# Performance work log

Measured on AMD Instinct MI355X. Metric: run time of the kernel, lower is better.

Reference implementation:

```python
import jax, jax.numpy as jnp
import numpy as np

E, H, I, T = 8, 1024, 4096, 8192  # experts, hidden, intermediate, total tokens


def setup_inputs() -> dict:
    key = jax.random.key(0)
    k1, k2, k3 = jax.random.split(key, 3)
    hiddens = jax.random.normal(k1, (T, H), dtype=jnp.float32)
    # expert weights, scaled like standard init
    w1_weight = jax.random.normal(k2, (E, H, I), dtype=jnp.float32) * (1.0 / np.sqrt(H).astype(np.float32))
    w2_weight = jax.random.normal(k3, (E, I, H), dtype=jnp.float32) * (1.0 / np.sqrt(I).astype(np.float32))
    # tokens are pre-grouped by expert; equal load of T//E tokens per expert
    batch_sizes = jnp.full((E,), T // E, dtype=jnp.int32)
    return {"hiddens": hiddens, "batch_sizes": batch_sizes,
            "w1_weight": w1_weight, "w2_weight": w2_weight}


def _gmm(x, w, batch_sizes):
    """Grouped matmul: rows of x are grouped contiguously by expert.
    x: [T, K], w: [E, K, N], batch_sizes: [E] (sums to T). Returns [T, N].
    Loop is over the small fixed expert count; each iteration is a dense
    GEMM with rows outside the expert's segment masked to zero.
    """
    n_experts = w.shape[0]
    ends = jnp.cumsum(batch_sizes)
    starts = ends - batch_sizes
    tok = jnp.arange(x.shape[0])[:, None]  # [T, 1]
    out = jnp.zeros((x.shape[0], w.shape[2]), dtype=x.dtype)
    for e in range(n_experts):
        mask = (tok >= starts[e]) & (tok < ends[e])  # [T, 1]
        out = out + jnp.where(mask, x, jnp.zeros((), x.dtype)) @ w[e]
    return out


def reference(hiddens, batch_sizes, w1_weight, w2_weight):
    up = _gmm(hiddens, w1_weight, batch_sizes)    # [T, I]
    down = _gmm(up, w2_weight, batch_sizes)       # [T, H]
    return down
```

## Files before the change

### kernel.cpp

```cpp
#include <hip/hip_runtime.h>
#include <hip/hip_bf16.h>


typedef unsigned short u16;
typedef unsigned int u32;
typedef __attribute__((ext_vector_type(8))) short bf16x8;
typedef __attribute__((ext_vector_type(4))) float f32x4;
typedef __attribute__((ext_vector_type(4))) u32 u32x4;

#define E_N 8
#define H_N 1024
#define I_N 4096
#define T_N 8192

#define GLD2LDS16(g, l)                                                        \
  __builtin_amdgcn_global_load_lds(                                            \
      (const __attribute__((address_space(1))) void*)(g),                      \
      (__attribute__((address_space(3))) void*)(l), 16, 0, 0)

__device__ __forceinline__ u16 f2bf(float f) {
  __hip_bfloat16 h = __float2bfloat16(f);
  return *(reinterpret_cast<u16*>(&h));
}

__device__ __forceinline__ u32 pkbf(float lo, float hi) {
  u32 a = __float_as_uint(lo) + 0x8000u;
  u32 b = __float_as_uint(hi) + 0x8000u;
  return __builtin_amdgcn_perm(b, a, 0x07060302u);
}

__global__ __launch_bounds__(256) void wgemm_kernel(const float* __restrict__ w1,
                                                    const float* __restrict__ w2,
                                                    u16* __restrict__ mt) {
  __shared__ u16 ldsA[4096];
  __shared__ u16 ldsB[4096];

  const int tid = threadIdx.x;
  const int lane = tid & 63;
  const int wv = tid >> 6;
  const int wm = wv >> 1, wn = wv & 1;
  const int lm = lane & 15, quad = lane >> 4;

  const int e = blockIdx.y;
  const int bm = blockIdx.x >> 3, bn = blockIdx.x & 7;
  const int row0 = bm * 128;
  const int col0 = bn * 128;

  const float* w1e = w1 + (size_t)e * H_N * I_N;
  const float* w2e = w2 + (size_t)e * I_N * H_N;
  u16* mte = mt + (size_t)e * H_N * H_N;

  const int a_mp = lane * 2;
  const float* gA0 = w2e + (size_t)(8 * wv) * H_N + row0 + a_mp;

  const int b_r = tid >> 2;
  const int b_k = (tid & 3) * 8;
  const float* gB0 = w1e + (size_t)(col0 + b_r) * I_N + b_k;
  const float* gB1 = gB0 + (size_t)64 * I_N;
  u16* ldsB_w = ldsB + b_r * 32 + b_k;

  f32x4 acc[4][4];
#pragma unroll
  for (int i = 0; i < 4; i++)
#pragma unroll
    for (int j = 0; j < 4; j++) acc[i][j] = (f32x4){0.f, 0.f, 0.f, 0.f};

  for (int k0 = 0; k0 < I_N; k0 += 32) {
    float2 va[8];
    const float* gA = gA0 + (size_t)k0 * H_N;
#pragma unroll
    for (int kk = 0; kk < 8; kk++)
      va[kk] = *(const float2*)(gA + (size_t)kk * H_N);

    float4 f0 = *(const float4*)(gB0 + k0);
    float4 f1 = *(const float4*)(gB0 + k0 + 4);
    float4 f2 = *(const float4*)(gB1 + k0);
    float4 f3 = *(const float4*)(gB1 + k0 + 4);

    u32 evn[4], odd[4];
#pragma unroll
    for (int j = 0; j < 4; j++) {
      evn[j] = pkbf(va[2 * j].x, va[2 * j + 1].x);
      odd[j] = pkbf(va[2 * j].y, va[2 * j + 1].y);
    }
    *(u32x4*)(ldsA + wv * 1024 + a_mp * 8) =
        (u32x4){evn[0], evn[1], evn[2], evn[3]};
    *(u32x4*)(ldsA + wv * 1024 + (a_mp + 1) * 8) =
        (u32x4){odd[0], odd[1], odd[2], odd[3]};

    *(u32x4*)ldsB_w = (u32x4){pkbf(f0.x, f0.y), pkbf(f0.z, f0.w),
                              pkbf(f1.x, f1.y), pkbf(f1.z, f1.w)};
    *(u32x4*)(ldsB_w + 64 * 32) = (u32x4){pkbf(f2.x, f2.y), pkbf(f2.z, f2.w),
                                          pkbf(f3.x, f3.y), pkbf(f3.z, f3.w)};

    __syncthreads();

    bf16x8 af[4], bfr[4];
#pragma unroll
    for (int mi = 0; mi < 4; mi++)
      af[mi] = *(const bf16x8*)(ldsA + quad * 1024 + (wm * 64 + mi * 16 + lm) * 8);
#pragma unroll
    for (int ni = 0; ni < 4; ni++)
      bfr[ni] = *(const bf16x8*)(ldsB + (wn * 64 + ni * 16 + lm) * 32 + quad * 8);
#pragma unroll
    for (int mi = 0; mi < 4; mi++)
#pragma unroll
      for (int ni = 0; ni < 4; ni++)
        acc[mi][ni] = __builtin_amdgcn_mfma_f32_16x16x32_bf16(
            af[mi], bfr[ni], acc[mi][ni], 0, 0, 0);

    __syncthreads();
  }

  const int orow = row0 + wm * 64 + quad * 4;
  const int ocol = col0 + wn * 64 + lm;
#pragma unroll
  for (int mi = 0; mi < 4; mi++)
#pragma unroll
    for (int ni = 0; ni < 4; ni++)
#pragma unroll
      for (int r = 0; r < 4; r++)
        mte[(size_t)(orow + mi * 16 + r) * H_N + ocol + ni * 16] =
            f2bf(acc[mi][ni][r]);
}

__global__ __launch_bounds__(256) void tgemm_kernel(const float* __restrict__ x,
                                                    const int* __restrict__ bsz,
                                                    const u16* __restrict__ mt,
                                                    float* __restrict__ out) {
  __shared__ u16 ldsA[4096];
  __shared__ u16 ldsB[4096];

  const int tid = threadIdx.x;
  const int lane = tid & 63;
  const int wv = tid >> 6;
  const int wm = wv >> 1, wn = wv & 1;
  const int lm = lane & 15, quad = lane >> 4;

  const int bm = blockIdx.x >> 3, bn = blockIdx.x & 7;
  const int row0 = bm * 128;
  const int col0 = bn * 128;

  int e = 0, start = 0;
#pragma unroll
  for (int i = 0; i < E_N; i++) {
    int b = bsz[i];
    if (row0 >= start + b) { start += b; e = i + 1; }
  }
  const u16* mte = mt + (size_t)e * H_N * H_N;

  const int s_r = tid >> 2;
  const int s_k = (tid & 3) * 8;
  const float* gA0 = x + (size_t)(row0 + s_r) * H_N + s_k;
  const float* gA1 = gA0 + (size_t)64 * H_N;
  const u16* gB0 = mte + (size_t)(col0 + s_r) * H_N + s_k;
  const u16* gB1 = gB0 + (size_t)64 * H_N;
  u16* ldsA_w = ldsA + s_r * 32 + s_k;
  u16* ldsB_dst = ldsB + wv * 512;

  f32x4 acc[4][4];
#pragma unroll
  for (int i = 0; i < 4; i++)
#pragma unroll
    for (int j = 0; j < 4; j++) acc[i][j] = (f32x4){0.f, 0.f, 0.f, 0.f};

  for (int k0 = 0; k0 < H_N; k0 += 32) {
    GLD2LDS16(gB0 + k0, ldsB_dst);
    GLD2LDS16(gB1 + k0, ldsB_dst + 2048);

    float4 f0 = *(const float4*)(gA0 + k0);
    float4 f1 = *(const float4*)(gA0 + k0 + 4);
    float4 f2 = *(const float4*)(gA1 + k0);
    float4 f3 = *(const float4*)(gA1 + k0 + 4);
    *(u32x4*)ldsA_w = (u32x4){pkbf(f0.x, f0.y), pkbf(f0.z, f0.w),
                              pkbf(f1.x, f1.y), pkbf(f1.z, f1.w)};
    *(u32x4*)(ldsA_w + 64 * 32) = (u32x4){pkbf(f2.x, f2.y), pkbf(f2.z, f2.w),
                                          pkbf(f3.x, f3.y), pkbf(f3.z, f3.w)};

    __syncthreads();

    bf16x8 af[4], bfr[4];
#pragma unroll
    for (int mi = 0; mi < 4; mi++)
      af[mi] = *(const bf16x8*)(ldsA + (wm * 64 + mi * 16 + lm) * 32 + quad * 8);
#pragma unroll
    for (int ni = 0; ni < 4; ni++)
      bfr[ni] = *(const bf16x8*)(ldsB + (wn * 64 + ni * 16 + lm) * 32 + quad * 8);
#pragma unroll
    for (int mi = 0; mi < 4; mi++)
#pragma unroll
      for (int ni = 0; ni < 4; ni++)
        acc[mi][ni] = __builtin_amdgcn_mfma_f32_16x16x32_bf16(
            af[mi], bfr[ni], acc[mi][ni], 0, 0, 0);

    __syncthreads();
  }

  const int orow = row0 + wm * 64 + quad * 4;
  const int ocol = col0 + wn * 64 + lm;
#pragma unroll
  for (int mi = 0; mi < 4; mi++)
#pragma unroll
    for (int ni = 0; ni < 4; ni++)
#pragma unroll
      for (int r = 0; r < 4; r++)
        out[(size_t)(orow + mi * 16 + r) * H_N + ocol + ni * 16] =
            acc[mi][ni][r];
}

extern "C" void kernel_launch(void* const* d_in, const int* in_sizes, int n_in,
                              void* d_out, int out_size, void* d_ws,
                              size_t ws_size, hipStream_t stream) {
  (void)in_sizes; (void)n_in; (void)out_size; (void)ws_size;
  const float* hiddens = (const float*)d_in[0];
  const int* bsz = (const int*)d_in[1];
  const float* w1 = (const float*)d_in[2];
  const float* w2 = (const float*)d_in[3];
  float* out = (float*)d_out;
  u16* mt = (u16*)d_ws;

  wgemm_kernel<<<dim3(64, E_N), 256, 0, stream>>>(w1, w2, mt);
  tgemm_kernel<<<dim3(512), 256, 0, stream>>>(hiddens, bsz, mt, out);
}
```

Before: 487.3 us.

## Pre-convert weights and activations to bf16 and use direct global-to-LDS loads

Adds separate conversion kernels that turn w1 and hiddens into bf16 and transpose-convert w2 into a K-contiguous bf16 layout in workspace. Both GEMM kernels can then load A and B tiles with global_load_lds instead of loading fp32 through registers and packing in the main loop. This removes repeated fp32 reads (each weight tile was re-read by 8 blocks) and in-loop conversion work. In exchange it adds three extra launches and a full fp32 read plus bf16 write of all weights per call, and it needs roughly 160 MB of workspace.

```diff
diff --git a/kernel.cpp b/kernel.cpp
--- a/kernel.cpp
+++ b/kernel.cpp
@@ -18,19 +18,68 @@
       (const __attribute__((address_space(1))) void*)(g),                      \
       (__attribute__((address_space(3))) void*)(l), 16, 0, 0)
 
-__device__ __forceinline__ u16 f2bf(float f) {
-  __hip_bfloat16 h = __float2bfloat16(f);
-  return *(reinterpret_cast<u16*>(&h));
-}
-
 __device__ __forceinline__ u32 pkbf(float lo, float hi) {
   u32 a = __float_as_uint(lo) + 0x8000u;
   u32 b = __float_as_uint(hi) + 0x8000u;
   return __builtin_amdgcn_perm(b, a, 0x07060302u);
 }
 
-__global__ __launch_bounds__(256) void wgemm_kernel(const float* __restrict__ w1,
-                                                    const float* __restrict__ w2,
+__device__ __forceinline__ u16 f2bf(float f) {
+  __hip_bfloat16 h = __float2bfloat16(f);
+  return *(reinterpret_cast<u16*>(&h));
+}
+
+__global__ __launch_bounds__(256) void cvt_kernel(const float* __restrict__ src,
+                                                  u16* __restrict__ dst) {
+  const size_t i = ((size_t)blockIdx.x * 256 + threadIdx.x) * 8;
+  float4 a = *(const float4*)(src + i);
+  float4 b = *(const float4*)(src + i + 4);
+  *(u32x4*)(dst + i) = (u32x4){pkbf(a.x, a.y), pkbf(a.z, a.w),
+                               pkbf(b.x, b.y), pkbf(b.z, b.w)};
+}
+
+__global__ __launch_bounds__(256) void transp_kernel(const float* __restrict__ w2,
+                                                     u16* __restrict__ w2t) {
+  __shared__ float tile[64 * 65];
+  const int tid = threadIdx.x;
+  const int h0 = blockIdx.x * 64;
+  const int i0 = blockIdx.y * 64;
+  const float* src = w2 + (size_t)blockIdx.z * I_N * H_N;
+  u16* dst = w2t + (size_t)blockIdx.z * H_N * I_N;
+
+  {
+    const int r = tid >> 4;
+    const int c4 = (tid & 15) * 4;
+#pragma unroll
+    for (int rr = 0; rr < 4; rr++) {
+      const int row = rr * 16 + r;
+      float4 v = *(const float4*)(src + (size_t)(i0 + row) * H_N + h0 + c4);
+      tile[row * 65 + c4 + 0] = v.x;
+      tile[row * 65 + c4 + 1] = v.y;
+      tile[row * 65 + c4 + 2] = v.z;
+      tile[row * 65 + c4 + 3] = v.w;
+    }
+  }
+  __syncthreads();
+
+  {
+    const int hr = tid >> 3;
+    const int ic = (tid & 7) * 8;
+#pragma unroll
+    for (int hh = 0; hh < 2; hh++) {
+      const int h = hh * 32 + hr;
+      u32 p[4];
+#pragma unroll
+      for (int j = 0; j < 4; j++)
+        p[j] = pkbf(tile[(ic + 2 * j) * 65 + h], tile[(ic + 2 * j + 1) * 65 + h]);
+      *(u32x4*)(dst + (size_t)(h0 + h) * I_N + i0 + ic) =
+          (u32x4){p[0], p[1], p[2], p[3]};
+    }
+  }
+}
+
+__global__ __launch_bounds__(256) void wgemm_kernel(const u16* __restrict__ w2t,
+                                                    const u16* __restrict__ w1b,
                                                     u16* __restrict__ mt) {
   __shared__ u16 ldsA[4096];
   __shared__ u16 ldsB[4096];
@@ -41,23 +90,23 @@
   const int wm = wv >> 1, wn = wv & 1;
   const int lm = lane & 15, quad = lane >> 4;
 
-  const int e = blockIdx.y;
-  const int bm = blockIdx.x >> 3, bn = blockIdx.x & 7;
-  const int row0 = bm * 128;
-  const int col0 = bn * 128;
-
-  const float* w1e = w1 + (size_t)e * H_N * I_N;
-  const float* w2e = w2 + (size_t)e * I_N * H_N;
+  const int e = blockIdx.x >> 6;
+  const int t = blockIdx.x & 63;
+  const int row0 = (t >> 3) * 128;
+  const int col0 = (t & 7) * 128;
+
+  const u16* Ae = w2t + (size_t)e * H_N * I_N;
+  const u16* Be = w1b + (size_t)e * H_N * I_N;
   u16* mte = mt + (size_t)e * H_N * H_N;
 
-  const int a_mp = lane * 2;
-  const float* gA0 = w2e + (size_t)(8 * wv) * H_N + row0 + a_mp;
-
-  const int b_r = tid >> 2;
-  const int b_k = (tid & 3) * 8;
-  const float* gB0 = w1e + (size_t)(col0 + b_r) * I_N + b_k;
-  const float* gB1 = gB0 + (size_t)64 * I_N;
-  u16* ldsB_w = ldsB + b_r * 32 + b_k;
+  const int s_r = tid >> 2;
+  const int s_k = (tid & 3) * 8;
+  const u16* gA0 = Ae + (size_t)(row0 + s_r) * I_N + s_k;
+  const u16* gA1 = gA0 + (size_t)64 * I_N;
+  const u16* gB0 = Be + (size_t)(col0 + s_r) * I_N + s_k;
+  const u16* gB1 = gB0 + (size_t)64 * I_N;
+  u16* ldsA_dst = ldsA + wv * 512;
+  u16* ldsB_dst = ldsB + wv * 512;
 
   f32x4 acc[4][4];
 #pragma unroll
@@ -66,39 +115,17 @@
     for (int j = 0; j < 4; j++) acc[i][j] = (f32x4){0.f, 0.f, 0.f, 0.f};
 
   for (int k0 = 0; k0 < I_N; k0 += 32) {
-    float2 va[8];
-    const float* gA = gA0 + (size_t)k0 * H_N;
-#pragma unroll
-    for (int kk = 0; kk < 8; kk++)
-      va[kk] = *(const float2*)(gA + (size_t)kk * H_N);
-
-    float4 f0 = *(const float4*)(gB0 + k0);
-    float4 f1 = *(const float4*)(gB0 + k0 + 4);
-    float4 f2 = *(const float4*)(gB1 + k0);
-    float4 f3 = *(const float4*)(gB1 + k0 + 4);
-
-    u32 evn[4], odd[4];
-#pragma unroll
-    for (int j = 0; j < 4; j++) {
-      evn[j] = pkbf(va[2 * j].x, va[2 * j + 1].x);
-      odd[j] = pkbf(va[2 * j].y, va[2 * j + 1].y);
-    }
-    *(u32x4*)(ldsA + wv * 1024 + a_mp * 8) =
-        (u32x4){evn[0], evn[1], evn[2], evn[3]};
-    *(u32x4*)(ldsA + wv * 1024 + (a_mp + 1) * 8) =
-        (u32x4){odd[0], odd[1], odd[2], odd[3]};
-
-    *(u32x4*)ldsB_w = (u32x4){pkbf(f0.x, f0.y), pkbf(f0.z, f0.w),
-                              pkbf(f1.x, f1.y), pkbf(f1.z, f1.w)};
-    *(u32x4*)(ldsB_w + 64 * 32) = (u32x4){pkbf(f2.x, f2.y), pkbf(f2.z, f2.w),
-                                          pkbf(f3.x, f3.y), pkbf(f3.z, f3.w)};
+    GLD2LDS16(gA0 + k0, ldsA_dst);
+    GLD2LDS16(gA1 + k0, ldsA_dst + 2048);
+    GLD2LDS16(gB0 + k0, ldsB_dst);
+    GLD2LDS16(gB1 + k0, ldsB_dst + 2048);
 
     __syncthreads();
 
     bf16x8 af[4], bfr[4];
 #pragma unroll
     for (int mi = 0; mi < 4; mi++)
-      af[mi] = *(const bf16x8*)(ldsA + quad * 1024 + (wm * 64 + mi * 16 + lm) * 8);
+      af[mi] = *(const bf16x8*)(ldsA + (wm * 64 + mi * 16 + lm) * 32 + quad * 8);
 #pragma unroll
     for (int ni = 0; ni < 4; ni++)
       bfr[ni] = *(const bf16x8*)(ldsB + (wn * 64 + ni * 16 + lm) * 32 + quad * 8);
@@ -124,7 +151,7 @@
             f2bf(acc[mi][ni][r]);
 }
 
-__global__ __launch_bounds__(256) void tgemm_kernel(const float* __restrict__ x,
+__global__ __launch_bounds__(256) void tgemm_kernel(const u16* __restrict__ xb,
                                                     const int* __restrict__ bsz,
                                                     const u16* __restrict__ mt,
                                                     float* __restrict__ out) {
@@ -151,11 +178,11 @@
 
   const int s_r = tid >> 2;
   const int s_k = (tid & 3) * 8;
-  const float* gA0 = x + (size_t)(row0 + s_r) * H_N + s_k;
-  const float* gA1 = gA0 + (size_t)64 * H_N;
+  const u16* gA0 = xb + (size_t)(row0 + s_r) * H_N + s_k;
+  const u16* gA1 = gA0 + (size_t)64 * H_N;
   const u16* gB0 = mte + (size_t)(col0 + s_r) * H_N + s_k;
   const u16* gB1 = gB0 + (size_t)64 * H_N;
-  u16* ldsA_w = ldsA + s_r * 32 + s_k;
+  u16* ldsA_dst = ldsA + wv * 512;
   u16* ldsB_dst = ldsB + wv * 512;
 
   f32x4 acc[4][4];
@@ -165,17 +192,10 @@
     for (int j = 0; j < 4; j++) acc[i][j] = (f32x4){0.f, 0.f, 0.f, 0.f};
 
   for (int k0 = 0; k0 < H_N; k0 += 32) {
+    GLD2LDS16(gA0 + k0, ldsA_dst);
+    GLD2LDS16(gA1 + k0, ldsA_dst + 2048);
     GLD2LDS16(gB0 + k0, ldsB_dst);
     GLD2LDS16(gB1 + k0, ldsB_dst + 2048);
-
-    float4 f0 = *(const float4*)(gA0 + k0);
-    float4 f1 = *(const float4*)(gA0 + k0 + 4);
-    float4 f2 = *(const float4*)(gA1 + k0);
-    float4 f3 = *(const float4*)(gA1 + k0 + 4);
-    *(u32x4*)ldsA_w = (u32x4){pkbf(f0.x, f0.y), pkbf(f0.z, f0.w),
-                              pkbf(f1.x, f1.y), pkbf(f1.z, f1.w)};
-    *(u32x4*)(ldsA_w + 64 * 32) = (u32x4){pkbf(f2.x, f2.y), pkbf(f2.z, f2.w),
-                                          pkbf(f3.x, f3.y), pkbf(f3.z, f3.w)};
 
     __syncthreads();
 
@@ -217,8 +237,17 @@
   const float* w1 = (const float*)d_in[2];
   const float* w2 = (const float*)d_in[3];
   float* out = (float*)d_out;
-  u16* mt = (u16*)d_ws;
-
-  wgemm_kernel<<<dim3(64, E_N), 256, 0, stream>>>(w1, w2, mt);
-  tgemm_kernel<<<dim3(512), 256, 0, stream>>>(hiddens, bsz, mt, out);
-}
+
+  char* ws = (char*)d_ws;
+  u16* w1b = (u16*)(ws);
+  u16* w2t = (u16*)(ws + (size_t)64 * 1024 * 1024);
+  u16* xb  = (u16*)(ws + (size_t)128 * 1024 * 1024);
+  u16* mt  = (u16*)(ws + (size_t)144 * 1024 * 1024);
+
+  cvt_kernel<<<dim3(16384), 256, 0, stream>>>(w1, w1b);
+  cvt_kernel<<<dim3(4096), 256, 0, stream>>>(hiddens, xb);
+  transp_kernel<<<dim3(16, 64, E_N), 256, 0, stream>>>(w2, w2t);
+
+  wgemm_kernel<<<dim3(512), 256, 0, stream>>>(w2t, w1b, mt);
+  tgemm_kernel<<<dim3(512), 256, 0, stream>>>(xb, bsz, mt, out);
+}
```

Result: no change. 483.7 us (-0.8%).
